# Optimization experiments

Hardware: AMD Instinct MI355X
Metric: run time of the kernel (lower is better)

The kernel has to match this reference:

```python
import jax, jax.numpy as jnp
import numpy as np

N_LVL = 127  # 8-bit symmetric: levels in [-128, 127]
BN_EPS = 1e-5


def ste_round(x):
    # straight-through estimator round (HAWQ uses STE for quantization)
    return x + jax.lax.stop_gradient(jnp.round(x) - x)


def quant_act(x):
    # symmetric per-tensor 8-bit activation quantization (QuantAct)
    s = jax.lax.stop_gradient(jnp.max(jnp.abs(x))) / N_LVL
    xq = jnp.clip(ste_round(x / s), -N_LVL - 1, N_LVL) * s
    return xq, s


def q_incept_conv(x, a_sf, w, g, b, m, v, stride, pad):
    # QuantBnConv2d: fold BN into conv, per-out-channel symmetric int8 weights
    std = jnp.sqrt(v + BN_EPS)
    wf = w * (g / std)[:, None, None, None]          # folded weight [O,I,kh,kw]
    bf = b - g * m / std                              # folded bias  [O]
    w_sf = jax.lax.stop_gradient(jnp.max(jnp.abs(wf), axis=(1, 2, 3))) / N_LVL
    wq = jnp.clip(ste_round(wf / w_sf[:, None, None, None]), -N_LVL - 1, N_LVL) * w_sf[:, None, None, None]
    conv_sf = a_sf * w_sf                             # per-channel output scale
    bq = ste_round(bf / conv_sf) * conv_sf            # bias quantized to conv scale
    y = jax.lax.conv_general_dilated(
        x, wq, window_strides=(stride, stride), padding=pad,
        dimension_numbers=('NCHW', 'OIHW', 'NCHW'))
    y = jax.nn.relu(y + bq[None, :, None, None])
    return quant_act(y)  # requantize activation (QuantAct with pre-scale)


def setup_inputs() -> dict:
    key = jax.random.key(0)
    ks = jax.random.split(key, 32)
    d = {}
    d['x'] = jax.random.normal(ks[0], (64, 384, 17, 17), jnp.float32)
    shapes = {
        'w1': (448, 384, 1, 1), 'w2': (384, 448, 3, 3),
        'w3': (384, 384, 1, 3), 'w4': (384, 384, 3, 1),
    }
    chans = {'1': 448, '2': 384, '3': 384, '4': 384}
    i = 1
    for idx in ['1', '2', '3', '4']:
        c = chans[idx]
        d['w' + idx] = jax.random.normal(ks[i], shapes['w' + idx], jnp.float32) * 0.05; i += 1
        d['g' + idx] = jax.random.uniform(ks[i], (c,), jnp.float32, 0.5, 1.5); i += 1
        d['b' + idx] = jax.random.normal(ks[i], (c,), jnp.float32) * 0.1; i += 1
        d['m' + idx] = jax.random.normal(ks[i], (c,), jnp.float32) * 0.1; i += 1
        d['v' + idx] = jax.random.uniform(ks[i], (c,), jnp.float32, 0.5, 1.5); i += 1
    return d


def reference(x, w1, g1, b1, m1, v1, w2, g2, b2, m2, v2,
              w3, g3, b3, m3, v3, w4, g4, b4, m4, v4):
    # q_input_act
    x, a_sf = quant_act(x)
    # conv_list: conv1 (1x1, 384->448), conv2 (3x3, 448->384, pad 1)
    x, a_sf = q_incept_conv(x, a_sf, w1, g1, b1, m1, v1, 1, [(0, 0), (0, 0)])
    x, a_sf = q_incept_conv(x, a_sf, w2, g2, b2, m2, v2, 1, [(1, 1), (1, 1)])
    # parallel branches
    y1, s1 = q_incept_conv(x, a_sf, w3, g3, b3, m3, v3, 1, [(0, 0), (1, 1)])  # 1x3
    y2, s2 = q_incept_conv(x, a_sf, w4, g4, b4, m4, v4, 1, [(1, 1), (0, 0)])  # 3x1
    # concat + rescaling requant (q_rescaling_activ): both branches already
    # dequantized floats; requantize to a single common scale
    cat = jnp.concatenate([y1, y2], axis=1)  # [N, 768, H, W]
    out, _ = quant_act(cat)
    return out
```

## Files before the change

### kernel.cpp

```cpp
#include <hip/hip_runtime.h>
#include <stdint.h>

#define NLVL 127.0f
#define NPOS (64 * 289)

typedef int v4i __attribute__((ext_vector_type(4)));
typedef int v16i __attribute__((ext_vector_type(16)));
typedef unsigned int uint;

__device__ __forceinline__ int swz_wg(int bid, int nwg) {
    const int q = nwg >> 3, r = nwg & 7;
    const int xcd = bid & 7;
    const int base = xcd < r ? xcd * (q + 1) : r * (q + 1) + (xcd - r) * q;
    return base + (bid >> 3);
}

__global__ __launch_bounds__(256) void amax_abs_kernel(const float* __restrict__ x,
                                                       int n, float* __restrict__ slot) {
    __shared__ float red[256];
    float lm = 0.f;
    for (int i = blockIdx.x * 256 + threadIdx.x; i < n; i += gridDim.x * 256)
        lm = fmaxf(lm, fabsf(x[i]));
    red[threadIdx.x] = lm;
    __syncthreads();
    for (int s = 128; s > 0; s >>= 1) {
        if (threadIdx.x < s) red[threadIdx.x] = fmaxf(red[threadIdx.x], red[threadIdx.x + s]);
        __syncthreads();
    }
    if (threadIdx.x == 0) atomicMax((unsigned int*)slot, __float_as_uint(red[0]));
}

__global__ __launch_bounds__(256) void quant_x_kernel(const float* __restrict__ x,
                                                      signed char* __restrict__ n0,
                                                      const float* __restrict__ scal) {
    __shared__ uint t32[64][97];
    const float s = scal[0] / NLVL;
    const int tid = threadIdx.x;
    const int pi = tid & 63;
    const int pos = blockIdx.x * 64 + pi;
    const int n = pos / 289;
    const int hw = pos - n * 289;
    const float* xb = x + (size_t)n * 384 * 289 + hw;
    for (int cq = tid >> 6; cq < 96; cq += 4) {
        uint pk = 0;
#pragma unroll
        for (int k = 0; k < 4; ++k) {
            const float f = xb[(size_t)(cq * 4 + k) * 289];
            float q = rintf(f / s);
            q = fminf(fmaxf(q, -128.f), 127.f);
            pk |= ((uint)((int)q & 0xff)) << (8 * k);
        }
        t32[pi][cq] = pk;
    }
    __syncthreads();
    for (int k = 0; k < 6; ++k) {
        const int c16 = (tid >> 6) + k * 4;
        uint4 v;
        v.x = t32[pi][c16 * 4 + 0];
        v.y = t32[pi][c16 * 4 + 1];
        v.z = t32[pi][c16 * 4 + 2];
        v.w = t32[pi][c16 * 4 + 3];
        *(uint4*)&n0[((size_t)c16 * NPOS + pos) * 16] = v;
    }
}

__global__ __launch_bounds__(256) void wq_kernel(
    const float* __restrict__ w1, const float* __restrict__ g1, const float* __restrict__ b1,
    const float* __restrict__ m1, const float* __restrict__ v1, signed char* __restrict__ s1w,
    float* __restrict__ s1sf, float* __restrict__ s1bf,
    const float* __restrict__ w2, const float* __restrict__ g2, const float* __restrict__ b2,
    const float* __restrict__ m2, const float* __restrict__ v2, signed char* __restrict__ s2w,
    float* __restrict__ s2sf, float* __restrict__ s2bf,
    const float* __restrict__ w3, const float* __restrict__ g3, const float* __restrict__ b3,
    const float* __restrict__ m3, const float* __restrict__ v3, signed char* __restrict__ s3w,
    float* __restrict__ s3sf, float* __restrict__ s3bf,
    const float* __restrict__ w4, const float* __restrict__ g4, const float* __restrict__ b4,
    const float* __restrict__ m4, const float* __restrict__ v4, signed char* __restrict__ s4w,
    float* __restrict__ s4sf, float* __restrict__ s4bf) {
    const int bid = blockIdx.x;
    const float *w, *g, *b, *m, *v;
    signed char* wstg;
    float *wsf, *bfv;
    int I, KHW, OCP, GPT, o;
    if (bid < 448) {
        w = w1; g = g1; b = b1; m = m1; v = v1; wstg = s1w; wsf = s1sf; bfv = s1bf;
        I = 384; KHW = 1; OCP = 512; GPT = 24; o = bid;
    } else if (bid < 832) {
        w = w2; g = g2; b = b2; m = m2; v = v2; wstg = s2w; wsf = s2sf; bfv = s2bf;
        I = 448; KHW = 9; OCP = 384; GPT = 28; o = bid - 448;
    } else if (bid < 1216) {
        w = w3; g = g3; b = b3; m = m3; v = v3; wstg = s3w; wsf = s3sf; bfv = s3bf;
        I = 384; KHW = 3; OCP = 384; GPT = 24; o = bid - 832;
    } else {
        w = w4; g = g4; b = b4; m = m4; v = v4; wstg = s4w; wsf = s4sf; bfv = s4bf;
        I = 384; KHW = 3; OCP = 384; GPT = 24; o = bid - 1216;
    }
    const int E = I * KHW;
    __shared__ float red[256];
    const float std_ = sqrtf(v[o] + 1e-5f);
    const float fac = g[o] / std_;
    float lm = 0.f;
    for (int e = threadIdx.x; e < E; e += 256)
        lm = fmaxf(lm, fabsf(w[(size_t)o * E + e] * fac));
    red[threadIdx.x] = lm;
    __syncthreads();
    for (int s = 128; s > 0; s >>= 1) {
        if (threadIdx.x < s) red[threadIdx.x] = fmaxf(red[threadIdx.x], red[threadIdx.x + s]);
        __syncthreads();
    }
    const float w_sf = red[0] / NLVL;
    for (int e = threadIdx.x; e < E; e += 256) {
        const float wf = w[(size_t)o * E + e] * fac;
        float q = rintf(wf / w_sf);
        q = fminf(fmaxf(q, -128.f), 127.f);
        const int i = e / KHW;
        const int r = e - i * KHW;
        wstg[((size_t)(r * GPT + (i >> 4)) * OCP + o) * 16 + (i & 15)] = (signed char)q;
    }
    if (threadIdx.x == 0) {
        wsf[o] = w_sf;
        bfv[o] = b[o] - g[o] * m[o] / std_;
    }
}

template <int CINP, int COUT, int OCP, int KH, int KW, int PH, int PW>
__global__ __launch_bounds__(256) void qconv_mfma(
    const signed char* __restrict__ xin, const signed char* __restrict__ wstg,
    const float* __restrict__ wsf, const float* __restrict__ bfv,
    const float* __restrict__ scal, int sidx,
    float* __restrict__ yout, float* __restrict__ amax_slot,
    const signed char* __restrict__ zero16, int coff16) {
    constexpr int KCN = CINP / 64;
    constexpr int GPT = CINP / 16;
    constexpr int NKT = KH * KW * KCN;
    static_assert(NKT % 3 == 0, "depth-3 rotation needs NKT % 3 == 0");
    constexpr int NOC = OCP / 128;
    constexpr int NPB = 145;
    __shared__ float red[256];

    const int tid = threadIdx.x;
    const int lane = tid & 63;
    const int wid = tid >> 6;
    const int l31 = lane & 31;
    const int lh = lane >> 5;

    const int wgid = swz_wg(blockIdx.x, NPB * NOC);
    const int pb = wgid / NOC;
    const int ob = wgid - pb * NOC;
    const int p_blk = pb * 128;
    const int oc_blk = ob * 128;

    int pn[2], ph_[2], pw_[2];
    bool prowok[2];
#pragma unroll
    for (int it = 0; it < 2; ++it) {
        const int myp = p_blk + (wid >> 1) * 64 + it * 32 + l31;
        prowok[it] = myp < NPOS;
        const int pc = prowok[it] ? myp : 0;
        pn[it] = pc / 289;
        const int hw = pc - pn[it] * 289;
        ph_[it] = hw / 17;
        pw_[it] = hw - ph_[it] * 17;
    }
    const int oc_col0 = oc_blk + (wid & 1) * 64 + l31;

    auto loadA = [&](int kt, v4i (&a)[2][2]) {
        const int tap = kt / KCN;
        const int kc = kt - tap * KCN;
        const int kh = tap / KW;
        const int kw = tap - kh * KW;
#pragma unroll
        for (int it = 0; it < 2; ++it) {
            const int ih = ph_[it] + kh - PH;
            const int iw = pw_[it] + kw - PW;
            const bool ok = prowok[it] & ((unsigned)ih < 17u) & ((unsigned)iw < 17u);
            const int spos = pn[it] * 289 + ih * 17 + iw;
#pragma unroll
            for (int ks = 0; ks < 2; ++ks) {
                const signed char* p =
                    ok ? xin + ((size_t)((kc * 4 + ks * 2 + lh) * NPOS + spos)) * 16 : zero16;
                a[ks][it] = *(const v4i*)p;
            }
        }
    };
    auto loadB = [&](int kt, v4i (&b)[2][2]) {
        const int tap = kt / KCN;
        const int kc = kt - tap * KCN;
        const signed char* base =
            wstg + ((size_t)(tap * GPT + kc * 4 + lh) * OCP + oc_col0) * 16;
        b[0][0] = *(const v4i*)(base);
        b[0][1] = *(const v4i*)(base + 32 * 16);
        b[1][0] = *(const v4i*)(base + (size_t)2 * OCP * 16);
        b[1][1] = *(const v4i*)(base + (size_t)2 * OCP * 16 + 32 * 16);
    };

    v16i acc[2][2] = {};

    auto compute = [&](const v4i (&a)[2][2], const v4i (&b)[2][2]) {
#pragma unroll
        for (int ks = 0; ks < 2; ++ks) {
            acc[0][0] = __builtin_amdgcn_mfma_i32_32x32x32_i8(a[ks][0], b[ks][0], acc[0][0], 0, 0, 0);
            acc[0][1] = __builtin_amdgcn_mfma_i32_32x32x32_i8(a[ks][0], b[ks][1], acc[0][1], 0, 0, 0);
            acc[1][0] = __builtin_amdgcn_mfma_i32_32x32x32_i8(a[ks][1], b[ks][0], acc[1][0], 0, 0, 0);
            acc[1][1] = __builtin_amdgcn_mfma_i32_32x32x32_i8(a[ks][1], b[ks][1], acc[1][1], 0, 0, 0);
        }
    };

    v4i aA[2][2], bA[2][2], aB[2][2], bB[2][2], aC[2][2], bC[2][2];
    loadA(0, aA); loadB(0, bA);
    loadA(1, aB); loadB(1, bB);
    loadA(2, aC); loadB(2, bC);
    for (int kt = 0; kt < NKT; kt += 3) {
        compute(aA, bA);
        if (kt + 3 < NKT) { loadA(kt + 3, aA); loadB(kt + 3, bA); }
        compute(aB, bB);
        if (kt + 4 < NKT) { loadA(kt + 4, aB); loadB(kt + 4, bB); }
        compute(aC, bC);
        if (kt + 5 < NKT) { loadA(kt + 5, aC); loadB(kt + 5, bC); }
    }

    const float a_sf = scal[sidx] / NLVL;
    float csf[2];
    int bb[2], ocv[2];
#pragma unroll
    for (int jt = 0; jt < 2; ++jt) {
        const int oc = oc_blk + (wid & 1) * 64 + jt * 32 + l31;
        ocv[jt] = oc;
        const bool real = oc < COUT;
        const float wsfv = real ? wsf[oc] : 0.f;
        csf[jt] = a_sf * wsfv;
        bb[jt] = real ? (int)rintf(bfv[oc] / csf[jt]) : 0;
    }
    float lm = 0.f;
#pragma unroll
    for (int it = 0; it < 2; ++it) {
#pragma unroll
        for (int reg = 0; reg < 16; ++reg) {
            const int prow_o =
                p_blk + (wid >> 1) * 64 + it * 32 + (reg & 3) + 8 * (reg >> 2) + 4 * lh;
            const bool pok = prow_o < NPOS;
#pragma unroll
            for (int jt = 0; jt < 2; ++jt) {
                int t2 = acc[it][jt][reg] + bb[jt];
                t2 = t2 > 0 ? t2 : 0;
                const float v2 = csf[jt] * (float)t2;
                if (pok && ocv[jt] < COUT) {
                    lm = fmaxf(lm, v2);
                    yout[((size_t)(coff16 + (ocv[jt] >> 4)) * NPOS + prow_o) * 16 +
                         (ocv[jt] & 15)] = v2;
                }
            }
        }
    }
    red[tid] = lm;
    __syncthreads();
    for (int s = 128; s > 0; s >>= 1) {
        if (tid < s) red[tid] = fmaxf(red[tid], red[tid + s]);
        __syncthreads();
    }
    if (tid == 0) atomicMax((unsigned int*)amax_slot, __float_as_uint(red[0]));
}

__global__ __launch_bounds__(256) void qconv_br34(
    const signed char* __restrict__ xin,
    const signed char* __restrict__ wstg3, const signed char* __restrict__ wstg4,
    const float* __restrict__ wsf3, const float* __restrict__ bf3,
    const float* __restrict__ wsf4, const float* __restrict__ bf4,
    const float* __restrict__ scal, int sidx,
    float* __restrict__ yout, float* __restrict__ amax_slot,
    const signed char* __restrict__ zero16) {
    constexpr int KCN = 6;
    constexpr int GPT = 24;
    constexpr int OCP = 384;
    constexpr int COUT = 384;
    constexpr int NKT = 18;
    constexpr int NOC = 3;
    constexpr int NPB = 145;
    __shared__ float red[256];

    const int tid = threadIdx.x;
    const int lane = tid & 63;
    const int wid = tid >> 6;
    const int l31 = lane & 31;
    const int lh = lane >> 5;

    const int wk = swz_wg(blockIdx.x, NPB * NOC * 2);
    const int br = wk & 1;
    const int pair = wk >> 1;
    const int pb = pair / NOC;
    const int ob = pair - pb * NOC;
    const int p_blk = pb * 128;
    const int oc_blk = ob * 128;

    const signed char* wstg = br ? wstg4 : wstg3;
    const float* wsf = br ? wsf4 : wsf3;
    const float* bfv = br ? bf4 : bf3;
    const int coff16 = br ? 24 : 0;

    int pn[2], ph_[2], pw_[2];
    bool prowok[2];
#pragma unroll
    for (int it = 0; it < 2; ++it) {
        const int myp = p_blk + (wid >> 1) * 64 + it * 32 + l31;
        prowok[it] = myp < NPOS;
        const int pc = prowok[it] ? myp : 0;
        pn[it] = pc / 289;
        const int hw = pc - pn[it] * 289;
        ph_[it] = hw / 17;
        pw_[it] = hw - ph_[it] * 17;
    }
    const int oc_col0 = oc_blk + (wid & 1) * 64 + l31;

    auto loadA = [&](int kt, v4i (&a)[2][2]) {
        const int tap = kt / KCN;
        const int kc = kt - tap * KCN;
        const int dh = br ? (tap - 1) : 0;
        const int dw = br ? 0 : (tap - 1);
#pragma unroll
        for (int it = 0; it < 2; ++it) {
            const int ih = ph_[it] + dh;
            const int iw = pw_[it] + dw;
            const bool ok = prowok[it] & ((unsigned)ih < 17u) & ((unsigned)iw < 17u);
            const int spos = pn[it] * 289 + ih * 17 + iw;
#pragma unroll
            for (int ks = 0; ks < 2; ++ks) {
                const signed char* p =
                    ok ? xin + ((size_t)((kc * 4 + ks * 2 + lh) * NPOS + spos)) * 16 : zero16;
                a[ks][it] = *(const v4i*)p;
            }
        }
    };
    auto loadB = [&](int kt, v4i (&b)[2][2]) {
        const int tap = kt / KCN;
        const int kc = kt - tap * KCN;
        const signed char* base =
            wstg + ((size_t)(tap * GPT + kc * 4 + lh) * OCP + oc_col0) * 16;
        b[0][0] = *(const v4i*)(base);
        b[0][1] = *(const v4i*)(base + 32 * 16);
        b[1][0] = *(const v4i*)(base + (size_t)2 * OCP * 16);
        b[1][1] = *(const v4i*)(base + (size_t)2 * OCP * 16 + 32 * 16);
    };

    v16i acc[2][2] = {};

    auto compute = [&](const v4i (&a)[2][2], const v4i (&b)[2][2]) {
#pragma unroll
        for (int ks = 0; ks < 2; ++ks) {
            acc[0][0] = __builtin_amdgcn_mfma_i32_32x32x32_i8(a[ks][0], b[ks][0], acc[0][0], 0, 0, 0);
            acc[0][1] = __builtin_amdgcn_mfma_i32_32x32x32_i8(a[ks][0], b[ks][1], acc[0][1], 0, 0, 0);
            acc[1][0] = __builtin_amdgcn_mfma_i32_32x32x32_i8(a[ks][1], b[ks][0], acc[1][0], 0, 0, 0);
            acc[1][1] = __builtin_amdgcn_mfma_i32_32x32x32_i8(a[ks][1], b[ks][1], acc[1][1], 0, 0, 0);
        }
    };

    v4i aA[2][2], bA[2][2], aB[2][2], bB[2][2], aC[2][2], bC[2][2];
    loadA(0, aA); loadB(0, bA);
    loadA(1, aB); loadB(1, bB);
    loadA(2, aC); loadB(2, bC);
    for (int kt = 0; kt < NKT; kt += 3) {
        compute(aA, bA);
        if (kt + 3 < NKT) { loadA(kt + 3, aA); loadB(kt + 3, bA); }
        compute(aB, bB);
        if (kt + 4 < NKT) { loadA(kt + 4, aB); loadB(kt + 4, bB); }
        compute(aC, bC);
        if (kt + 5 < NKT) { loadA(kt + 5, aC); loadB(kt + 5, bC); }
    }

    const float a_sf = scal[sidx] / NLVL;
    float csf[2];
    int bb[2], ocv[2];
#pragma unroll
    for (int jt = 0; jt < 2; ++jt) {
        const int oc = oc_blk + (wid & 1) * 64 + jt * 32 + l31;
        ocv[jt] = oc;
        csf[jt] = a_sf * wsf[oc];
        bb[jt] = (int)rintf(bfv[oc] / csf[jt]);
    }
    float lm = 0.f;
#pragma unroll
    for (int it = 0; it < 2; ++it) {
#pragma unroll
        for (int reg = 0; reg < 16; ++reg) {
            const int prow_o =
                p_blk + (wid >> 1) * 64 + it * 32 + (reg & 3) + 8 * (reg >> 2) + 4 * lh;
            const bool pok = prow_o < NPOS;
#pragma unroll
            for (int jt = 0; jt < 2; ++jt) {
                int t2 = acc[it][jt][reg] + bb[jt];
                t2 = t2 > 0 ? t2 : 0;
                const float v2 = csf[jt] * (float)t2;
                if (pok) {
                    lm = fmaxf(lm, v2);
                    yout[((size_t)(coff16 + (ocv[jt] >> 4)) * NPOS + prow_o) * 16 +
                         (ocv[jt] & 15)] = v2;
                }
            }
        }
    }
    red[tid] = lm;
    __syncthreads();
    for (int s = 128; s > 0; s >>= 1) {
        if (tid < s) red[tid] = fmaxf(red[tid], red[tid + s]);
        __syncthreads();
    }
    if (tid == 0) atomicMax((unsigned int*)amax_slot, __float_as_uint(red[0]));
}

__global__ __launch_bounds__(256) void requant_kernel(const float* __restrict__ f,
                                                      signed char* __restrict__ q,
                                                      const float* __restrict__ scal,
                                                      int idx, int nvec) {
    const float s = scal[idx] / NLVL;
    for (int i = blockIdx.x * 256 + threadIdx.x; i < nvec; i += gridDim.x * 256) {
        const float4 v = ((const float4*)f)[i];
        const int b0 = (int)fminf(fmaxf(rintf(v.x / s), -128.f), 127.f);
        const int b1 = (int)fminf(fmaxf(rintf(v.y / s), -128.f), 127.f);
        const int b2 = (int)fminf(fmaxf(rintf(v.z / s), -128.f), 127.f);
        const int b3 = (int)fminf(fmaxf(rintf(v.w / s), -128.f), 127.f);
        ((unsigned int*)q)[i] =
            (b0 & 0xff) | ((b1 & 0xff) << 8) | ((b2 & 0xff) << 16) | ((b3 & 0xff) << 24);
    }
}

__global__ __launch_bounds__(256) void transpose_requant_kernel(
    const float* __restrict__ f, float* __restrict__ out,
    const float* __restrict__ scal, int idx) {
    __shared__ float tile[64][65];
    const float s = scal[idx] / NLVL;
    const int tid = threadIdx.x;
    const int w = tid >> 6, l = tid & 63;
    const int pt = blockIdx.x % 289, ct = blockIdx.x / 289;
    const int pos0 = pt * 64, c0 = ct * 64;
    const int slab = ct * 4 + w;
#pragma unroll
    for (int j = 0; j < 4; ++j) {
        const int p = (l >> 2) + j * 16;
        const int co = (l & 3) * 4;
        const float4 v = *(const float4*)&f[((size_t)slab * NPOS + pos0 + p) * 16 + co];
        tile[p][w * 16 + co + 0] = v.x;
        tile[p][w * 16 + co + 1] = v.y;
        tile[p][w * 16 + co + 2] = v.z;
        tile[p][w * 16 + co + 3] = v.w;
    }
    __syncthreads();
    const int pos = pos0 + l;
    const int n = pos / 289;
    const int hw = pos - n * 289;
#pragma unroll
    for (int k = 0; k < 16; ++k) {
        const int c = c0 + w * 16 + k;
        float v = tile[l][w * 16 + k];
        v = fminf(fmaxf(rintf(v / s), -128.f), 127.f) * s;
        out[((size_t)(n * 768 + c)) * 289 + hw] = v;
    }
}

extern "C" void kernel_launch(void* const* d_in, const int* in_sizes, int n_in,
                              void* d_out, int out_size, void* d_ws, size_t ws_size,
                              hipStream_t stream) {
    const float* x  = (const float*)d_in[0];
    const float* w1 = (const float*)d_in[1];
    const float* g1 = (const float*)d_in[2];
    const float* b1 = (const float*)d_in[3];
    const float* m1 = (const float*)d_in[4];
    const float* v1 = (const float*)d_in[5];
    const float* w2 = (const float*)d_in[6];
    const float* g2 = (const float*)d_in[7];
    const float* b2 = (const float*)d_in[8];
    const float* m2 = (const float*)d_in[9];
    const float* v2 = (const float*)d_in[10];
    const float* w3 = (const float*)d_in[11];
    const float* g3 = (const float*)d_in[12];
    const float* b3 = (const float*)d_in[13];
    const float* m3 = (const float*)d_in[14];
    const float* v3 = (const float*)d_in[15];
    const float* w4 = (const float*)d_in[16];
    const float* g4 = (const float*)d_in[17];
    const float* b4 = (const float*)d_in[18];
    const float* m4 = (const float*)d_in[19];
    const float* v4 = (const float*)d_in[20];
    float* out = (float*)d_out;
    char* ws = (char*)d_ws;

    size_t off = 0;
    auto take = [&](size_t bytes) {
        char* p = ws + off;
        off = (off + bytes + 255) & ~(size_t)255;
        return p;
    };
    float* scal = (float*)take(64);
    const signed char* zero16 = (const signed char*)(scal + 8);
    signed char* wstg1 = (signed char*)take((size_t)24 * 512 * 16);
    float* sf1 = (float*)take(448 * 4);
    float* bf1 = (float*)take(448 * 4);
    signed char* wstg2 = (signed char*)take((size_t)9 * 28 * 384 * 16);
    float* sf2 = (float*)take(384 * 4);
    float* bf2 = (float*)take(384 * 4);
    signed char* wstg3 = (signed char*)take((size_t)3 * 24 * 384 * 16);
    float* sf3 = (float*)take(384 * 4);
    float* bf3 = (float*)take(384 * 4);
    signed char* wstg4 = (signed char*)take((size_t)3 * 24 * 384 * 16);
    float* sf4 = (float*)take(384 * 4);
    float* bf4 = (float*)take(384 * 4);
    signed char* n0 = (signed char*)take((size_t)24 * NPOS * 16);
    signed char* q1 = (signed char*)take((size_t)28 * NPOS * 16);
    signed char* q2 = (signed char*)take((size_t)24 * NPOS * 16);
    float* fbuf = (float*)take((size_t)48 * NPOS * 16 * 4);

    hipMemsetAsync(scal, 0, 64, stream);
    hipMemsetAsync(wstg1, 0, (size_t)24 * 512 * 16, stream);

    wq_kernel<<<1600, 256, 0, stream>>>(w1, g1, b1, m1, v1, wstg1, sf1, bf1,
                                        w2, g2, b2, m2, v2, wstg2, sf2, bf2,
                                        w3, g3, b3, m3, v3, wstg3, sf3, bf3,
                                        w4, g4, b4, m4, v4, wstg4, sf4, bf4);

    amax_abs_kernel<<<1024, 256, 0, stream>>>(x, 64 * 384 * 289, scal + 0);
    quant_x_kernel<<<289, 256, 0, stream>>>(x, n0, scal);

    qconv_mfma<384, 448, 512, 1, 1, 0, 0>
        <<<145 * 4, 256, 0, stream>>>(n0, wstg1, sf1, bf1, scal, 0, fbuf, scal + 1, zero16, 0);
    requant_kernel<<<2048, 256, 0, stream>>>(fbuf, q1, scal, 1, 28 * NPOS * 16 / 4);

    qconv_mfma<448, 384, 384, 3, 3, 1, 1>
        <<<145 * 3, 256, 0, stream>>>(q1, wstg2, sf2, bf2, scal, 1, fbuf, scal + 2, zero16, 0);
    requant_kernel<<<2048, 256, 0, stream>>>(fbuf, q2, scal, 2, 24 * NPOS * 16 / 4);

    qconv_br34<<<145 * 3 * 2, 256, 0, stream>>>(q2, wstg3, wstg4, sf3, bf3, sf4, bf4,
                                                scal, 2, fbuf, scal + 3, zero16);

    transpose_requant_kernel<<<289 * 12, 256, 0, stream>>>(fbuf, out, scal, 3);
}
```

Measured before the change: 225.8 us.

## Split conv2 K-loop across two workgroups with int32 partials and combine kernel

The 3x3 conv2 (448->384) was launched with 435 workgroups, which underfills the GPU. It now splits the 63 K-tiles into two halves (33 and 30), each written as int32 partial sums into separate halves of fbuf. A new combine kernel adds the partials, applies the quantized bias, ReLU and scale, and tracks the amax. The branch-3/4 kernel is refactored into templated bodies with compile-time tap geometry. This doubles the parallelism at the cost of an extra pass over roughly 28 MB of partial sums plus one more kernel launch.

```diff
diff --git a/kernel.cpp b/kernel.cpp
--- a/kernel.cpp
+++ b/kernel.cpp
@@ -261,22 +261,15 @@
     if (tid == 0) atomicMax((unsigned int*)amax_slot, __float_as_uint(red[0]));
 }
 
-__global__ __launch_bounds__(256) void qconv_br34(
-    const signed char* __restrict__ xin,
-    const signed char* __restrict__ wstg3, const signed char* __restrict__ wstg4,
-    const float* __restrict__ wsf3, const float* __restrict__ bf3,
-    const float* __restrict__ wsf4, const float* __restrict__ bf4,
-    const float* __restrict__ scal, int sidx,
-    float* __restrict__ yout, float* __restrict__ amax_slot,
-    const signed char* __restrict__ zero16) {
-    constexpr int KCN = 6;
-    constexpr int GPT = 24;
+template <int KT0, int KTN>
+__device__ __forceinline__ void conv2_body(
+    const signed char* __restrict__ xin, const signed char* __restrict__ wstg,
+    int* __restrict__ pout, const signed char* __restrict__ zero16, int pb, int ob) {
+    constexpr int KCN = 7;
+    constexpr int GPT = 28;
     constexpr int OCP = 384;
-    constexpr int COUT = 384;
-    constexpr int NKT = 18;
-    constexpr int NOC = 3;
-    constexpr int NPB = 145;
-    __shared__ float red[256];
+    constexpr int END = KT0 + KTN;
+    static_assert(KTN % 3 == 0, "depth-3 rotation needs KTN % 3 == 0");
 
     const int tid = threadIdx.x;
     const int lane = tid & 63;
@@ -284,18 +277,8 @@
     const int l31 = lane & 31;
     const int lh = lane >> 5;
 
-    const int wk = swz_wg(blockIdx.x, NPB * NOC * 2);
-    const int br = wk & 1;
-    const int pair = wk >> 1;
-    const int pb = pair / NOC;
-    const int ob = pair - pb * NOC;
     const int p_blk = pb * 128;
     const int oc_blk = ob * 128;
-
-    const signed char* wstg = br ? wstg4 : wstg3;
-    const float* wsf = br ? wsf4 : wsf3;
-    const float* bfv = br ? bf4 : bf3;
-    const int coff16 = br ? 24 : 0;
 
     int pn[2], ph_[2], pw_[2];
     bool prowok[2];
@@ -314,12 +297,178 @@
     auto loadA = [&](int kt, v4i (&a)[2][2]) {
         const int tap = kt / KCN;
         const int kc = kt - tap * KCN;
-        const int dh = br ? (tap - 1) : 0;
-        const int dw = br ? 0 : (tap - 1);
+        const int kh = tap / 3;
+        const int kw = tap - kh * 3;
 #pragma unroll
         for (int it = 0; it < 2; ++it) {
-            const int ih = ph_[it] + dh;
-            const int iw = pw_[it] + dw;
+            const int ih = ph_[it] + kh - 1;
+            const int iw = pw_[it] + kw - 1;
+            const bool ok = prowok[it] & ((unsigned)ih < 17u) & ((unsigned)iw < 17u);
+            const int spos = pn[it] * 289 + ih * 17 + iw;
+#pragma unroll
+            for (int ks = 0; ks < 2; ++ks) {
+                const signed char* p =
+                    ok ? xin + ((size_t)((kc * 4 + ks * 2 + lh) * NPOS + spos)) * 16 : zero16;
+                a[ks][it] = *(const v4i*)p;
+            }
+        }
+    };
+    auto loadB = [&](int kt, v4i (&b)[2][2]) {
+        const int tap = kt / KCN;
+        const int kc = kt - tap * KCN;
+        const signed char* base =
+            wstg + ((size_t)(tap * GPT + kc * 4 + lh) * OCP + oc_col0) * 16;
+        b[0][0] = *(const v4i*)(base);
+        b[0][1] = *(const v4i*)(base + 32 * 16);
+        b[1][0] = *(const v4i*)(base + (size_t)2 * OCP * 16);
+        b[1][1] = *(const v4i*)(base + (size_t)2 * OCP * 16 + 32 * 16);
+    };
+
+    v16i acc[2][2] = {};
+
+    auto compute = [&](const v4i (&a)[2][2], const v4i (&b)[2][2]) {
+#pragma unroll
+        for (int ks = 0; ks < 2; ++ks) {
+            acc[0][0] = __builtin_amdgcn_mfma_i32_32x32x32_i8(a[ks][0], b[ks][0], acc[0][0], 0, 0, 0);
+            acc[0][1] = __builtin_amdgcn_mfma_i32_32x32x32_i8(a[ks][0], b[ks][1], acc[0][1], 0, 0, 0);
+            acc[1][0] = __builtin_amdgcn_mfma_i32_32x32x32_i8(a[ks][1], b[ks][0], acc[1][0], 0, 0, 0);
+            acc[1][1] = __builtin_amdgcn_mfma_i32_32x32x32_i8(a[ks][1], b[ks][1], acc[1][1], 0, 0, 0);
+        }
+    };
+
+    v4i aA[2][2], bA[2][2], aB[2][2], bB[2][2], aC[2][2], bC[2][2];
+    loadA(KT0 + 0, aA); loadB(KT0 + 0, bA);
+    loadA(KT0 + 1, aB); loadB(KT0 + 1, bB);
+    loadA(KT0 + 2, aC); loadB(KT0 + 2, bC);
+    for (int kt = KT0; kt < END; kt += 3) {
+        compute(aA, bA);
+        if (kt + 3 < END) { loadA(kt + 3, aA); loadB(kt + 3, bA); }
+        compute(aB, bB);
+        if (kt + 4 < END) { loadA(kt + 4, aB); loadB(kt + 4, bB); }
+        compute(aC, bC);
+        if (kt + 5 < END) { loadA(kt + 5, aC); loadB(kt + 5, bC); }
+    }
+
+#pragma unroll
+    for (int it = 0; it < 2; ++it) {
+#pragma unroll
+        for (int reg = 0; reg < 16; ++reg) {
+            const int prow_o =
+                p_blk + (wid >> 1) * 64 + it * 32 + (reg & 3) + 8 * (reg >> 2) + 4 * lh;
+            if (prow_o < NPOS) {
+#pragma unroll
+                for (int jt = 0; jt < 2; ++jt) {
+                    const int oc = oc_blk + (wid & 1) * 64 + jt * 32 + l31;
+                    pout[((size_t)(oc >> 4) * NPOS + prow_o) * 16 + (oc & 15)] =
+                        acc[it][jt][reg];
+                }
+            }
+        }
+    }
+}
+
+__global__ __launch_bounds__(256) void qconv2_split(
+    const signed char* __restrict__ xin, const signed char* __restrict__ wstg,
+    int* __restrict__ p0, int* __restrict__ p1, const signed char* __restrict__ zero16) {
+    const int wk = swz_wg(blockIdx.x, 145 * 3 * 2);
+    const int kidx = wk & 1;
+    const int tile = wk >> 1;
+    const int pb = tile / 3;
+    const int ob = tile - pb * 3;
+    if (kidx == 0)
+        conv2_body<0, 33>(xin, wstg, p0, zero16, pb, ob);
+    else
+        conv2_body<33, 30>(xin, wstg, p1, zero16, pb, ob);
+}
+
+__global__ __launch_bounds__(256) void combine2_kernel(
+    int* pbuf0, const int* __restrict__ pbuf1,
+    const float* __restrict__ wsf, const float* __restrict__ bfv,
+    const float* __restrict__ scal, float* __restrict__ amax_slot) {
+    __shared__ float scsf[384];
+    __shared__ int sbq[384];
+    __shared__ float red[256];
+    const float a_sf = scal[1] / NLVL;
+    for (int o = threadIdx.x; o < 384; o += 256) {
+        const float c = a_sf * wsf[o];
+        scsf[o] = c;
+        sbq[o] = (int)rintf(bfv[o] / c);
+    }
+    __syncthreads();
+    const int nvec = 24 * NPOS * 16 / 4;
+    float lm = 0.f;
+    for (int i = blockIdx.x * 256 + threadIdx.x; i < nvec; i += gridDim.x * 256) {
+        const int4 a = ((const int4*)pbuf0)[i];
+        const int4 b = ((const int4*)pbuf1)[i];
+        const int idx = i * 4;
+        const int slab = idx / (NPOS * 16);
+        const int ocb = slab * 16 + (idx & 15);
+        int4 o;
+        int t;
+        float v;
+        t = a.x + b.x + sbq[ocb + 0]; t = t > 0 ? t : 0; v = scsf[ocb + 0] * (float)t;
+        lm = fmaxf(lm, v); o.x = __float_as_int(v);
+        t = a.y + b.y + sbq[ocb + 1]; t = t > 0 ? t : 0; v = scsf[ocb + 1] * (float)t;
+        lm = fmaxf(lm, v); o.y = __float_as_int(v);
+        t = a.z + b.z + sbq[ocb + 2]; t = t > 0 ? t : 0; v = scsf[ocb + 2] * (float)t;
+        lm = fmaxf(lm, v); o.z = __float_as_int(v);
+        t = a.w + b.w + sbq[ocb + 3]; t = t > 0 ? t : 0; v = scsf[ocb + 3] * (float)t;
+        lm = fmaxf(lm, v); o.w = __float_as_int(v);
+        ((int4*)pbuf0)[i] = o;
+    }
+    red[threadIdx.x] = lm;
+    __syncthreads();
+    for (int s = 128; s > 0; s >>= 1) {
+        if (threadIdx.x < s) red[threadIdx.x] = fmaxf(red[threadIdx.x], red[threadIdx.x + s]);
+        __syncthreads();
+    }
+    if (threadIdx.x == 0) atomicMax((unsigned int*)amax_slot, __float_as_uint(red[0]));
+}
+
+template <int KH, int KW, int PH, int PW>
+__device__ __forceinline__ float conv34_body(
+    const signed char* __restrict__ xin, const signed char* __restrict__ wstg,
+    const float* __restrict__ wsf, const float* __restrict__ bfv, float a_sf,
+    float* __restrict__ yout, const signed char* __restrict__ zero16,
+    int coff16, int pb, int ob) {
+    constexpr int KCN = 6;
+    constexpr int GPT = 24;
+    constexpr int OCP = 384;
+    constexpr int NKT = KH * KW * KCN;
+    static_assert(NKT % 3 == 0, "depth-3 rotation needs NKT % 3 == 0");
+
+    const int tid = threadIdx.x;
+    const int lane = tid & 63;
+    const int wid = tid >> 6;
+    const int l31 = lane & 31;
+    const int lh = lane >> 5;
+
+    const int p_blk = pb * 128;
+    const int oc_blk = ob * 128;
+
+    int pn[2], ph_[2], pw_[2];
+    bool prowok[2];
+#pragma unroll
+    for (int it = 0; it < 2; ++it) {
+        const int myp = p_blk + (wid >> 1) * 64 + it * 32 + l31;
+        prowok[it] = myp < NPOS;
+        const int pc = prowok[it] ? myp : 0;
+        pn[it] = pc / 289;
+        const int hw = pc - pn[it] * 289;
+        ph_[it] = hw / 17;
+        pw_[it] = hw - ph_[it] * 17;
+    }
+    const int oc_col0 = oc_blk + (wid & 1) * 64 + l31;
+
+    auto loadA = [&](int kt, v4i (&a)[2][2]) {
+        const int tap = kt / KCN;
+        const int kc = kt - tap * KCN;
+        const int kh = tap / KW;
+        const int kw = tap - kh * KW;
+#pragma unroll
+        for (int it = 0; it < 2; ++it) {
+            const int ih = ph_[it] + kh - PH;
+            const int iw = pw_[it] + kw - PW;
             const bool ok = prowok[it] & ((unsigned)ih < 17u) & ((unsigned)iw < 17u);
             const int spos = pn[it] * 289 + ih * 17 + iw;
 #pragma unroll
@@ -366,7 +515,6 @@
         if (kt + 5 < NKT) { loadA(kt + 5, aC); loadB(kt + 5, bC); }
     }
 
-    const float a_sf = scal[sidx] / NLVL;
     float csf[2];
     int bb[2], ocv[2];
 #pragma unroll
@@ -397,13 +545,35 @@
             }
         }
     }
-    red[tid] = lm;
+    return lm;
+}
+
+__global__ __launch_bounds__(256) void qconv34(
+    const signed char* __restrict__ xin,
+    const signed char* __restrict__ wstg3, const signed char* __restrict__ wstg4,
+    const float* __restrict__ sf3, const float* __restrict__ bf3,
+    const float* __restrict__ sf4, const float* __restrict__ bf4,
+    const float* __restrict__ scal, float* __restrict__ yout,
+    float* __restrict__ amax_slot, const signed char* __restrict__ zero16) {
+    __shared__ float red[256];
+    const int wk = swz_wg(blockIdx.x, 145 * 3 * 2);
+    const int br = wk & 1;
+    const int tile = wk >> 1;
+    const int pb = tile / 3;
+    const int ob = tile - pb * 3;
+    const float a_sf = scal[2] / NLVL;
+    float lm;
+    if (br == 0)
+        lm = conv34_body<1, 3, 0, 1>(xin, wstg3, sf3, bf3, a_sf, yout, zero16, 0, pb, ob);
+    else
+        lm = conv34_body<3, 1, 1, 0>(xin, wstg4, sf4, bf4, a_sf, yout, zero16, 24, pb, ob);
+    red[threadIdx.x] = lm;
     __syncthreads();
     for (int s = 128; s > 0; s >>= 1) {
-        if (tid < s) red[tid] = fmaxf(red[tid], red[tid + s]);
+        if (threadIdx.x < s) red[threadIdx.x] = fmaxf(red[threadIdx.x], red[threadIdx.x + s]);
         __syncthreads();
     }
-    if (tid == 0) atomicMax((unsigned int*)amax_slot, __float_as_uint(red[0]));
+    if (threadIdx.x == 0) atomicMax((unsigned int*)amax_slot, __float_as_uint(red[0]));
 }
 
 __global__ __launch_bounds__(256) void requant_kernel(const float* __restrict__ f,
@@ -507,6 +677,9 @@
     signed char* q2 = (signed char*)take((size_t)24 * NPOS * 16);
     float* fbuf = (float*)take((size_t)48 * NPOS * 16 * 4);
 
+    int* p0 = (int*)fbuf;
+    int* p1 = (int*)(fbuf + (size_t)24 * NPOS * 16);
+
     hipMemsetAsync(scal, 0, 64, stream);
     hipMemsetAsync(wstg1, 0, (size_t)24 * 512 * 16, stream);
 
@@ -522,12 +695,12 @@
         <<<145 * 4, 256, 0, stream>>>(n0, wstg1, sf1, bf1, scal, 0, fbuf, scal + 1, zero16, 0);
     requant_kernel<<<2048, 256, 0, stream>>>(fbuf, q1, scal, 1, 28 * NPOS * 16 / 4);
 
-    qconv_mfma<448, 384, 384, 3, 3, 1, 1>
-        <<<145 * 3, 256, 0, stream>>>(q1, wstg2, sf2, bf2, scal, 1, fbuf, scal + 2, zero16, 0);
+    qconv2_split<<<145 * 3 * 2, 256, 0, stream>>>(q1, wstg2, p0, p1, zero16);
+    combine2_kernel<<<2048, 256, 0, stream>>>(p0, p1, sf2, bf2, scal, scal + 2);
     requant_kernel<<<2048, 256, 0, stream>>>(fbuf, q2, scal, 2, 24 * NPOS * 16 / 4);
 
-    qconv_br34<<<145 * 3 * 2, 256, 0, stream>>>(q2, wstg3, wstg4, sf3, bf3, sf4, bf4,
-                                                scal, 2, fbuf, scal + 3, zero16);
+    qconv34<<<145 * 3 * 2, 256, 0, stream>>>(q2, wstg3, wstg4, sf3, bf3, sf4, bf4,
+                                             scal, fbuf, scal + 3, zero16);
 
     transpose_requant_kernel<<<289 * 12, 256, 0, stream>>>(fbuf, out, scal, 3);
 }
```

Measured after the change: 236.9 us. +4.9%, slower.
